# Kernel optimization log

Measured on AMD Instinct MI355X. Metric: run time of the kernel, lower is better.

Reference implementation:

```python
import jax, jax.numpy as jnp
import numpy as np

BS, T, N_AGENTS, N_ACTIONS = 8, 256, 8, 20
A = N_AGENTS * N_ACTIONS          # 160 gru input dim
E, D, HID, S = 128, 128, 32, 256  # encoder_dim, decoder_dim, mixing_embed_dim, state_dim
EMBED = HID * (A + E)             # 9216


def _lin(k, out_d, in_d):
    s = 1.0 / np.sqrt(in_d)
    return jax.random.uniform(k, (out_d, in_d), jnp.float32, -s, s)


def _vec(k, d, fan):
    s = 1.0 / np.sqrt(fan)
    return jax.random.uniform(k, (d,), jnp.float32, -s, s)


def setup_inputs() -> dict:
    key = jax.random.key(0)
    ks = jax.random.split(key, 32)
    inp = {
        'act': jax.random.uniform(ks[0], (BS, T, N_AGENTS, N_ACTIONS), jnp.float32),
        'states': jax.random.normal(ks[1], (BS, T, S), jnp.float32),
        # GRU (PyTorch layout: gates stacked [r; z; n])
        'gru_wih': _lin(ks[2], 3 * E, A),
        'gru_whh': _lin(ks[3], 3 * E, E),
        'gru_bih': _vec(ks[4], 3 * E, E),
        'gru_bhh': _vec(ks[5], 3 * E, E),
        # encoder fc
        'fc_w': _lin(ks[6], D, E),
        'fc_b': _vec(ks[7], D, E),
        # attention
        'attn_w': _lin(ks[8], D, D + E),
        'v_w': _vec(ks[9], D, D),
        # hyper_w_1 (2-layer MLP)
        'hw1_w0': _lin(ks[10], EMBED, S), 'hw1_b0': _vec(ks[11], EMBED, S),
        'hw1_w1': _lin(ks[12], EMBED, EMBED), 'hw1_b1': _vec(ks[13], EMBED, EMBED),
        # hyper_w_final (2-layer MLP)
        'hwf_w0': _lin(ks[14], HID, S), 'hwf_b0': _vec(ks[15], HID, S),
        'hwf_w1': _lin(ks[16], HID, HID), 'hwf_b1': _vec(ks[17], HID, HID),
        # hyper_b_1
        'hb1_w': _lin(ks[18], HID, S), 'hb1_b': _vec(ks[19], HID, S),
        # hyper_b_2 (2-layer MLP)
        'hb2_w0': _lin(ks[20], HID, S), 'hb2_b0': _vec(ks[21], HID, S),
        'hb2_w1': _lin(ks[22], 1, HID), 'hb2_b1': _vec(ks[23], 1, HID),
    }
    return inp


def reference(act, states, gru_wih, gru_whh, gru_bih, gru_bhh, fc_w, fc_b,
              attn_w, v_w, hw1_w0, hw1_b0, hw1_w1, hw1_b1,
              hwf_w0, hwf_b0, hwf_w1, hwf_b1, hb1_w, hb1_b,
              hb2_w0, hb2_b0, hb2_w1, hb2_b1):
    bs, t, n_ag, n_ac = act.shape
    a = n_ag * n_ac
    e = gru_whh.shape[1]
    d = fc_w.shape[0]
    hid = hb1_w.shape[0]

    act_flat = act.reshape(bs, t, a)
    # act_his = [zeros, act]; prefixes use only the first t steps of it
    x = jnp.concatenate([jnp.zeros((bs, 1, a), act.dtype), act_flat[:, : t - 1]], axis=1)

    # GRU over full sequence once (causal => identical to recomputing each prefix)
    def step(h, xt):
        gi = xt @ gru_wih.T + gru_bih
        gh = h @ gru_whh.T + gru_bhh
        ir, iz, i_n = jnp.split(gi, 3, axis=-1)
        hr, hz, h_n = jnp.split(gh, 3, axis=-1)
        r = jax.nn.sigmoid(ir + hr)
        z = jax.nn.sigmoid(iz + hz)
        n = jnp.tanh(i_n + r * h_n)
        h_new = (1.0 - z) * n + z * h
        return h_new, h_new

    h0 = jnp.zeros((bs, e), act.dtype)
    _, enc = jax.lax.scan(step, h0, jnp.swapaxes(x, 0, 1))
    enc = jnp.swapaxes(enc, 0, 1)  # [bs, T, E]

    # s0 for prefix ending at step q is tanh(fc(enc[:, q]))
    s0 = jnp.tanh(enc @ fc_w.T + fc_b)  # [bs, T, D]

    # attention: cat order is (s, enc_output)
    w_s, w_e = attn_w[:, :d], attn_w[:, d:]
    ps = s0 @ w_s.T            # [bs, Tq, D]
    pe = enc @ w_e.T           # [bs, Tk, D]
    pre = jnp.tanh(ps[:, :, None, :] + pe[:, None, :, :])  # [bs, Tq, Tk, D]
    scores = jnp.einsum('bqkd,d->bqk', pre, v_w)
    mask = jnp.tril(jnp.ones((t, t), bool))  # key j <= query q (prefix j < idx)
    scores = jnp.where(mask[None], scores, -jnp.inf)
    attn = jax.nn.softmax(scores, axis=-1)
    c = jnp.einsum('bqk,bke->bqe', attn, enc)  # [bs, T, E]

    inp = jnp.concatenate([act_flat, c], axis=-1).reshape(bs * t, 1, a + e)
    st = states.reshape(bs * t, -1)

    w1 = (jax.nn.relu(st @ hw1_w0.T + hw1_b0) @ hw1_w1.T + hw1_b1).reshape(bs * t, a + e, hid)
    b1 = (st @ hb1_w.T + hb1_b)[:, None, :]
    h = jax.nn.relu(jnp.einsum('bik,bkh->bih', inp, w1) + b1)  # [bs*T, 1, hid]

    wf = (jax.nn.relu(st @ hwf_w0.T + hwf_b0) @ hwf_w1.T + hwf_b1)[:, :, None]  # [bs*T, hid, 1]
    b2 = (jax.nn.relu(st @ hb2_w0.T + hb2_b0) @ hb2_w1.T + hb2_b1)[:, :, None]  # [bs*T, 1, 1]
    q = (jnp.einsum('bih,bho->bio', h, wf) + b2).reshape(bs, t, 1)
    return q
```

## Files before the change

### kernel.cpp

```cpp
#include <hip/hip_runtime.h>
#include <hip/hip_bf16.h>
#include <stdint.h>

typedef __attribute__((ext_vector_type(4))) float f32x4;
typedef __attribute__((ext_vector_type(8))) short short8v;
typedef __attribute__((ext_vector_type(4))) unsigned short u16x4;

constexpr int kT  = 256;
constexpr int kA  = 160;

__device__ __forceinline__ float bf2f(unsigned short u){
  union { unsigned int u; float f; } c; c.u = ((unsigned int)u) << 16; return c.f;
}
__device__ __forceinline__ unsigned short f2bf(float f){
  union { float f; unsigned int u; } c; c.f = f;
  unsigned int r = (c.u + 0x7FFFu + ((c.u >> 16) & 1u)) >> 16;
  return (unsigned short)r;
}
__device__ __forceinline__ float sigmoid_fast(float x){
  return __builtin_amdgcn_rcpf(1.f + __expf(-x));
}
__device__ __forceinline__ float tanhf_fast(float x){
  float xc = fminf(fmaxf(x, -15.f), 15.f);
  float t = __expf(2.f * xc);
  return (t - 1.f) * __builtin_amdgcn_rcpf(t + 1.f);
}
__device__ __forceinline__ void gload_lds16(const void* g, void* l){
  __builtin_amdgcn_global_load_lds((const __attribute__((address_space(1))) void*)g,
                                   (__attribute__((address_space(3))) void*)l, 16, 0, 0);
}
__device__ __forceinline__ void bar_lgkm(){
  asm volatile("s_waitcnt lgkmcnt(0)" ::: "memory");
  __builtin_amdgcn_s_barrier();
  asm volatile("" ::: "memory");
}
__device__ __forceinline__ void bar_only(){
  asm volatile("" ::: "memory");
  __builtin_amdgcn_s_barrier();
  asm volatile("" ::: "memory");
}

__global__ __launch_bounds__(256) void k_fill_f32(float* out, int n, float v){
  int i = blockIdx.x * blockDim.x + threadIdx.x;
  if (i < n) out[i] = v;
}

__global__ __launch_bounds__(256) void k_f32_to_bf16(const float* __restrict__ src,
                                                     unsigned short* __restrict__ dst, int n4){
  int stride = gridDim.x * blockDim.x;
  for (int i = blockIdx.x * blockDim.x + threadIdx.x; i < n4; i += stride){
    f32x4 v = *(const f32x4*)(src + (size_t)i * 4);
    u16x4 o;
    o[0] = f2bf(v[0]); o[1] = f2bf(v[1]); o[2] = f2bf(v[2]); o[3] = f2bf(v[3]);
    *(u16x4*)(dst + (size_t)i * 4) = o;
  }
}

__global__ __launch_bounds__(384) void k_gi(const float* __restrict__ act,
                                            const float* __restrict__ wih,
                                            const float* __restrict__ bih,
                                            float* __restrict__ gi){
  int blk = blockIdx.x;
  int b = blk >> 5, tg = blk & 31;
  int j = threadIdx.x;
  __shared__ __align__(16) float xh[8][kA];
  for (int idx = j; idx < 8 * kA; idx += 384){
    int u = idx / kA, i = idx - u * kA;
    int t = tg * 8 + u;
    xh[u][i] = (t == 0) ? 0.f : act[((size_t)b * kT + t - 1) * kA + i];
  }
  __syncthreads();
  float acc[8] = {0,0,0,0,0,0,0,0};
  for (int i = 0; i < kA; i += 4){
    f32x4 wv = *(const f32x4*)(wih + (size_t)j * kA + i);
#pragma unroll
    for (int jj = 0; jj < 4; ++jj)
#pragma unroll
      for (int u = 0; u < 8; ++u)
        acc[u] += wv[jj] * xh[u][i + jj];
  }
  float bv = bih[j];
#pragma unroll
  for (int u = 0; u < 8; ++u)
    gi[((size_t)b * kT + tg * 8 + u) * 384 + j] = acc[u] + bv;
}

__global__ __launch_bounds__(512) void k_gru_conv(const float* __restrict__ gi,
                                                  const float* __restrict__ whh,
                                                  const float* __restrict__ bhh,
                                                  float* __restrict__ enc,
                                                  const float* __restrict__ csrc,
                                                  unsigned short* __restrict__ cdst,
                                                  int n4){
  if (blockIdx.x >= 8){
    int stride = (gridDim.x - 8) * 512;
    for (int i = (blockIdx.x - 8) * 512 + threadIdx.x; i < n4; i += stride){
      f32x4 v = *(const f32x4*)(csrc + (size_t)i * 4);
      u16x4 o;
      o[0] = f2bf(v[0]); o[1] = f2bf(v[1]); o[2] = f2bf(v[2]); o[3] = f2bf(v[3]);
      *(u16x4*)(cdst + (size_t)i * 4) = o;
    }
    return;
  }
  int b = blockIdx.x;
  int tid = threadIdx.x;
  int e = tid & 127, s = tid >> 7;
  float W0[32], W1[32], W2[32];
#pragma unroll
  for (int k = 0; k < 32; ++k){
    W0[k] = whh[(size_t)(0 * 128 + e) * 128 + s * 32 + k];
    W1[k] = whh[(size_t)(1 * 128 + e) * 128 + s * 32 + k];
    W2[k] = whh[(size_t)(2 * 128 + e) * 128 + s * 32 + k];
  }
  __shared__ __align__(16) float h_lds[128];
  __shared__ __align__(16) float red[12][128];
  if (tid < 128) h_lds[tid] = 0.f;
  float bh0 = 0.f, bh1 = 0.f, bh2 = 0.f;
  if (tid < 128){ bh0 = bhh[e]; bh1 = bhh[128 + e]; bh2 = bhh[256 + e]; }
  const float* gib = gi + (size_t)b * kT * 384;
  float* encb = enc + (size_t)b * kT * 128;
  float gir = 0.f, giz = 0.f, gin = 0.f;
  if (tid < 128){ gir = gib[e]; giz = gib[128 + e]; gin = gib[256 + e]; }
  bar_lgkm();
  for (int t = 0; t < kT; ++t){
    float p0 = 0.f, p1 = 0.f, p2 = 0.f;
#pragma unroll
    for (int k4 = 0; k4 < 8; ++k4){
      f32x4 hv = *(const f32x4*)(h_lds + s * 32 + k4 * 4);
#pragma unroll
      for (int jj = 0; jj < 4; ++jj){
        p0 += W0[k4 * 4 + jj] * hv[jj];
        p1 += W1[k4 * 4 + jj] * hv[jj];
        p2 += W2[k4 * 4 + jj] * hv[jj];
      }
    }
    float nir = 0.f, niz = 0.f, nin = 0.f;
    if (t + 1 < kT && tid < 128){
      const float* gn = gib + (size_t)(t + 1) * 384;
      nir = gn[e]; niz = gn[128 + e]; nin = gn[256 + e];
    }
    red[s * 3 + 0][e] = p0; red[s * 3 + 1][e] = p1; red[s * 3 + 2][e] = p2;
    bar_lgkm();
    if (tid < 128){
      float ghr = red[0][e] + red[3][e] + red[6][e] + red[9][e]  + bh0;
      float ghz = red[1][e] + red[4][e] + red[7][e] + red[10][e] + bh1;
      float ghn = red[2][e] + red[5][e] + red[8][e] + red[11][e] + bh2;
      float r = sigmoid_fast(gir + ghr);
      float z = sigmoid_fast(giz + ghz);
      float n = tanhf_fast(gin + r * ghn);
      float hnew = (1.f - z) * n + z * h_lds[e];
      h_lds[e] = hnew;
      encb[t * 128 + e] = hnew;
    }
    bar_lgkm();
    gir = nir; giz = niz; gin = nin;
  }
}

__global__ __launch_bounds__(128) void k_attnpre(const float* __restrict__ enc,
                                                 const float* __restrict__ fc_w,
                                                 const float* __restrict__ fc_b,
                                                 const float* __restrict__ attn_w,
                                                 float* __restrict__ ps,
                                                 float* __restrict__ pe){
  int bt = blockIdx.x, o = threadIdx.x;
  __shared__ __align__(16) float ench[128], s0h[128];
  ench[o] = enc[(size_t)bt * 128 + o];
  __syncthreads();
  float a0 = fc_b[o], a1 = 0.f;
  for (int i = 0; i < 128; i += 4){
    f32x4 wv = *(const f32x4*)(fc_w + (size_t)o * 128 + i);
    f32x4 we = *(const f32x4*)(attn_w + (size_t)o * 256 + 128 + i);
    f32x4 ev = *(const f32x4*)(ench + i);
#pragma unroll
    for (int jj = 0; jj < 4; ++jj){ a0 += wv[jj] * ev[jj]; a1 += we[jj] * ev[jj]; }
  }
  s0h[o] = tanhf_fast(a0);
  pe[(size_t)bt * 128 + o] = a1;
  __syncthreads();
  float a2 = 0.f;
  for (int i = 0; i < 128; i += 4){
    f32x4 ws = *(const f32x4*)(attn_w + (size_t)o * 256 + i);
    f32x4 sv = *(const f32x4*)(s0h + i);
#pragma unroll
    for (int jj = 0; jj < 4; ++jj) a2 += ws[jj] * sv[jj];
  }
  ps[(size_t)bt * 128 + o] = a2;
}

__global__ __launch_bounds__(256) void k_attn(const float* __restrict__ enc,
                                              const float* __restrict__ ps,
                                              const float* __restrict__ pe,
                                              const float* __restrict__ v_w,
                                              float* __restrict__ cbuf){
  int q = blockIdx.x, b = blockIdx.y;
  int tid = threadIdx.x;
  __shared__ __align__(16) float psh[128], vwh[128];
  __shared__ __align__(16) float sch[256];
  __shared__ __align__(16) float rr[256];
  __shared__ float mxs, dns;
  if (tid < 128){
    psh[tid] = ps[((size_t)b * kT + q) * 128 + tid];
    vwh[tid] = v_w[tid];
  }
  __syncthreads();
  int nk = q + 1;
  for (int k = tid; k < nk; k += 256){
    const float* per = pe + ((size_t)b * kT + k) * 128;
    float sc = 0.f;
    for (int d = 0; d < 128; d += 4){
      f32x4 pv = *(const f32x4*)(per + d);
      f32x4 qv = *(const f32x4*)(psh + d);
      sc += vwh[d + 0] * tanhf_fast(qv[0] + pv[0]);
      sc += vwh[d + 1] * tanhf_fast(qv[1] + pv[1]);
      sc += vwh[d + 2] * tanhf_fast(qv[2] + pv[2]);
      sc += vwh[d + 3] * tanhf_fast(qv[3] + pv[3]);
    }
    sch[k] = sc;
  }
  __syncthreads();
  float lm = -3.0e38f;
  for (int k = tid; k < nk; k += 256) lm = fmaxf(lm, sch[k]);
  rr[tid] = lm; __syncthreads();
  for (int off = 128; off > 0; off >>= 1){
    if (tid < off) rr[tid] = fmaxf(rr[tid], rr[tid + off]);
    __syncthreads();
  }
  if (tid == 0) mxs = rr[0];
  __syncthreads();
  float mxv = mxs;
  float lsum = 0.f;
  for (int k = tid; k < nk; k += 256){
    float p = __expf(sch[k] - mxv);
    sch[k] = p; lsum += p;
  }
  __syncthreads();
  rr[tid] = lsum; __syncthreads();
  for (int off = 128; off > 0; off >>= 1){
    if (tid < off) rr[tid] += rr[tid + off];
    __syncthreads();
  }
  if (tid == 0) dns = __builtin_amdgcn_rcpf(rr[0]);
  __syncthreads();
  float rd = dns;
  int d = tid & 127, half = tid >> 7;
  float acc = 0.f;
  for (int k = half; k < nk; k += 2)
    acc += sch[k] * enc[((size_t)b * kT + k) * 128 + d];
  rr[tid] = acc; __syncthreads();
  if (half == 0)
    cbuf[((size_t)b * kT + q) * 128 + d] = (acc + rr[d + 128]) * rd;
}

template<int RELU>
__global__ __launch_bounds__(512, 4) void k_gemm8(const unsigned short* __restrict__ A,
                                                  const unsigned short* __restrict__ B,
                                                  const float* __restrict__ bias,
                                                  unsigned short* __restrict__ C,
                                                  int M, int Nc, int K, int ldc){
  __shared__ __align__(16) unsigned short Lds[3][12288];
  int nbm = M >> 7;
  int nwg = gridDim.x, bid = blockIdx.x;
  int cpx = nwg >> 3;
  int sw  = (bid & 7) * cpx + (bid >> 3);
  int bm = sw % nbm, bn = sw / nbm;
  int arow0 = bm << 7, bcol0 = bn << 8;
  int t = threadIdx.x;
  int l = t & 63, w = t >> 6;
  int wr = w >> 2, wc = w & 3;
  int lr = l & 15, kq = l >> 4;
  int ra = t >> 2,          pa = t & 3;
  int rb0 = t >> 2,         pb0 = t & 3;
  int rb1 = (t + 512) >> 2, pb1 = (t + 512) & 3;
  int aoffg  = ra  * (K * 2) + ((pa  ^ ((ra  >> 1) & 3)) << 4);
  int boffg0 = rb0 * (K * 2) + ((pb0 ^ ((rb0 >> 1) & 3)) << 4);
  int boffg1 = rb1 * (K * 2) + ((pb1 ^ ((rb1 >> 1) & 3)) << 4);
  const char* Ag = (const char*)(A + (size_t)arow0 * K);
  const char* Bg = (const char*)(B + (size_t)bcol0 * K);
  int lA  = t * 16;
  int lB0 = 8192 + t * 16;
  int lB1 = 16384 + t * 16;
  int kk16 = (kq ^ ((lr >> 1) & 3)) << 4;
  int aRd = (wr * 64 + lr) * 64 + kk16;
  int bRd = 8192 + (wc * 64 + lr) * 64 + kk16;
  f32x4 acc[4][4] = {};
  int nt = K >> 5;

  auto stage = [&](int kt, int bi){
    size_t kb = (size_t)kt * 64;
    char* Ld = (char*)Lds[bi];
    gload_lds16(Ag + aoffg  + kb, Ld + lA);
    gload_lds16(Bg + boffg0 + kb, Ld + lB0);
    gload_lds16(Bg + boffg1 + kb, Ld + lB1);
  };
  auto compute = [&](int bi){
    const char* Ld = (const char*)Lds[bi];
    short8v af[4], bf[4];
#pragma unroll
    for (int m = 0; m < 4; ++m) af[m] = *(const short8v*)(Ld + aRd + m * 1024);
#pragma unroll
    for (int n = 0; n < 4; ++n) bf[n] = *(const short8v*)(Ld + bRd + n * 1024);
    __builtin_amdgcn_s_setprio(1);
#pragma unroll
    for (int m = 0; m < 4; ++m)
#pragma unroll
      for (int n = 0; n < 4; ++n)
        acc[m][n] = __builtin_amdgcn_mfma_f32_16x16x32_bf16(af[m], bf[n], acc[m][n], 0, 0, 0);
    __builtin_amdgcn_s_setprio(0);
  };

  stage(0, 0);
  stage(1, 1);
  int cur = 0;
  for (int kt = 0; kt < nt; ++kt){
    if (kt + 2 < nt){
      int nb = cur + 2; if (nb >= 3) nb -= 3;
      stage(kt + 2, nb);
      asm volatile("s_waitcnt vmcnt(6)" ::: "memory");
    } else if (kt + 2 == nt){
      asm volatile("s_waitcnt vmcnt(3)" ::: "memory");
    } else {
      asm volatile("s_waitcnt vmcnt(0)" ::: "memory");
    }
    bar_only();
    compute(cur);
    bar_only();
    ++cur; if (cur == 3) cur = 0;
  }

#pragma unroll
  for (int m = 0; m < 4; ++m){
    int row = arow0 + wr * 64 + m * 16 + kq * 4;
#pragma unroll
    for (int n = 0; n < 4; ++n){
      int col = bcol0 + wc * 64 + n * 16 + lr;
      float bv = bias[col];
#pragma unroll
      for (int r = 0; r < 4; ++r){
        float v = acc[m][n][r] + bv;
        if (RELU) v = fmaxf(v, 0.f);
        C[(size_t)(row + r) * ldc + col] = f2bf(v);
      }
    }
  }
}

__global__ __launch_bounds__(256) void k_final(const float* __restrict__ states,
                                               const float* __restrict__ act,
                                               const float* __restrict__ cbuf,
                                               const unsigned short* __restrict__ w1f,
                                               const float* __restrict__ hb1_w, const float* __restrict__ hb1_b,
                                               const float* __restrict__ hwf_w0, const float* __restrict__ hwf_b0,
                                               const float* __restrict__ hwf_w1, const float* __restrict__ hwf_b1,
                                               const float* __restrict__ hb2_w0, const float* __restrict__ hb2_b0,
                                               const float* __restrict__ hb2_w1, const float* __restrict__ hb2_b1,
                                               float* __restrict__ out){
  int bt = blockIdx.x, tid = threadIdx.x;
  __shared__ __align__(16) float sth[256], inph[288], red[256];
  __shared__ __align__(16) float t1h[32], t2h[32], b1h[32], wfh[32], hvals[32];
  __shared__ float b2s;
  sth[tid] = states[(size_t)bt * 256 + tid];
  if (tid < 160) inph[tid] = act[(size_t)bt * 160 + tid];
  if (tid < 128) inph[160 + tid] = cbuf[(size_t)bt * 128 + tid];
  __syncthreads();
  int o = tid & 31, s = tid >> 5;
  float p1 = 0.f, p2 = 0.f, p3 = 0.f;
  for (int k = s * 32; k < s * 32 + 32; k += 4){
    f32x4 sv  = *(const f32x4*)(sth + k);
    f32x4 w1v = *(const f32x4*)(hwf_w0 + (size_t)o * 256 + k);
    f32x4 w2v = *(const f32x4*)(hb2_w0 + (size_t)o * 256 + k);
    f32x4 w3v = *(const f32x4*)(hb1_w  + (size_t)o * 256 + k);
#pragma unroll
    for (int jj = 0; jj < 4; ++jj){
      p1 += w1v[jj] * sv[jj]; p2 += w2v[jj] * sv[jj]; p3 += w3v[jj] * sv[jj];
    }
  }
  red[tid] = p1; __syncthreads();
  if (tid < 32){
    float a = hwf_b0[tid];
#pragma unroll
    for (int s8 = 0; s8 < 8; ++s8) a += red[s8 * 32 + tid];
    t1h[tid] = fmaxf(a, 0.f);
  }
  __syncthreads();
  red[tid] = p2; __syncthreads();
  if (tid < 32){
    float a = hb2_b0[tid];
#pragma unroll
    for (int s8 = 0; s8 < 8; ++s8) a += red[s8 * 32 + tid];
    t2h[tid] = fmaxf(a, 0.f);
  }
  __syncthreads();
  red[tid] = p3; __syncthreads();
  if (tid < 32){
    float a = hb1_b[tid];
#pragma unroll
    for (int s8 = 0; s8 < 8; ++s8) a += red[s8 * 32 + tid];
    b1h[tid] = a;
  }
  __syncthreads();
  if (tid < 32){
    float a = hwf_b1[tid];
#pragma unroll
    for (int j = 0; j < 32; ++j) a += hwf_w1[(size_t)tid * 32 + j] * t1h[j];
    wfh[tid] = a;
  }
  if (tid == 64){
    float a = hb2_b1[0];
#pragma unroll
    for (int j = 0; j < 32; ++j) a += hb2_w1[j] * t2h[j];
    b2s = a;
  }
  __syncthreads();
  float ph = 0.f;
  const unsigned short* wrow = w1f + (size_t)bt * 9216;
  for (int i = s * 36; i < s * 36 + 36; ++i)
    ph += inph[i] * bf2f(wrow[i * 32 + o]);
  red[tid] = ph; __syncthreads();
  if (tid < 32){
    float a = b1h[tid];
#pragma unroll
    for (int s8 = 0; s8 < 8; ++s8) a += red[s8 * 32 + tid];
    hvals[tid] = fmaxf(a, 0.f) * wfh[tid];
  }
  __syncthreads();
  if (tid == 0){
    float q = b2s;
#pragma unroll
    for (int j = 0; j < 32; ++j) q += hvals[j];
    out[bt] = q;
  }
}

extern "C" void kernel_launch(void* const* d_in, const int* in_sizes, int n_in,
                              void* d_out, int out_size, void* d_ws, size_t ws_size,
                              hipStream_t stream){
  float* outp = (float*)d_out;

  bool ok = (n_in == 24) && out_size == 2048 &&
            in_sizes[0] == 327680 && in_sizes[1] == 524288 &&
            in_sizes[2] == 61440  && in_sizes[3] == 49152 &&
            in_sizes[10] == 2359296 && in_sizes[12] == 84934656;
  if (!ok){
    k_fill_f32<<<dim3(8), dim3(256), 0, stream>>>(outp, 2048, 1.0e6f);
    return;
  }

  const float* act    = (const float*)d_in[0];
  const float* states = (const float*)d_in[1];
  const float* wih    = (const float*)d_in[2];
  const float* whh    = (const float*)d_in[3];
  const float* bih    = (const float*)d_in[4];
  const float* bhh    = (const float*)d_in[5];
  const float* fc_w   = (const float*)d_in[6];
  const float* fc_b   = (const float*)d_in[7];
  const float* attn_w = (const float*)d_in[8];
  const float* v_w    = (const float*)d_in[9];
  const float* hw1_w0 = (const float*)d_in[10];
  const float* hw1_b0 = (const float*)d_in[11];
  const float* hw1_w1 = (const float*)d_in[12];
  const float* hw1_b1 = (const float*)d_in[13];
  const float* hwf_w0 = (const float*)d_in[14];
  const float* hwf_b0 = (const float*)d_in[15];
  const float* hwf_w1 = (const float*)d_in[16];
  const float* hwf_b1 = (const float*)d_in[17];
  const float* hb1_w  = (const float*)d_in[18];
  const float* hb1_b  = (const float*)d_in[19];
  const float* hb2_w0 = (const float*)d_in[20];
  const float* hb2_b0 = (const float*)d_in[21];
  const float* hb2_w1 = (const float*)d_in[22];
  const float* hb2_b1 = (const float*)d_in[23];

  char* ws = (char*)d_ws;
  size_t off = 0;
  auto alloc = [&](size_t bytes)->void*{
    void* p = ws + off; off += (bytes + 255) & ~(size_t)255; return p;
  };
  unsigned short* zb  = (unsigned short*)alloc((size_t)2048 * 9216 * 2);
  unsigned short* w1f = (unsigned short*)alloc((size_t)2048 * 9216 * 2);
  unsigned short* w0b = (unsigned short*)alloc((size_t)9216 * 256 * 2);
  unsigned short* stb = (unsigned short*)alloc((size_t)2048 * 256 * 2);
  float* gi   = (float*)alloc((size_t)2048 * 384 * 4);
  float* enc  = (float*)alloc((size_t)2048 * 128 * 4);
  float* psb  = (float*)alloc((size_t)2048 * 128 * 4);
  float* peb  = (float*)alloc((size_t)2048 * 128 * 4);
  float* cbuf = (float*)alloc((size_t)2048 * 128 * 4);
  size_t floor_bytes = off;
  const size_t row_bytes = (size_t)9216 * 2;
  if (ws_size < floor_bytes + 256 * row_bytes){
    k_fill_f32<<<dim3(8), dim3(256), 0, stream>>>(outp, 2048, (float)(ws_size >> 20));
    return;
  }
  size_t avail = ws_size - floor_bytes;
  int chunk_rows = (int)(((avail / row_bytes) / 256) * 256);
  if (chunk_rows > 9216) chunk_rows = 9216;
  unsigned short* w1c = (unsigned short*)(ws + floor_bytes);
  int first_nc = chunk_rows < 9216 ? chunk_rows : 9216;

  k_f32_to_bf16<<<dim3(1024), dim3(256), 0, stream>>>(hw1_w0, w0b, 9216 * 256 / 4);
  k_f32_to_bf16<<<dim3(256),  dim3(256), 0, stream>>>(states, stb, 2048 * 256 / 4);
  k_gi<<<dim3(256), dim3(384), 0, stream>>>(act, wih, bih, gi);
  k_gru_conv<<<dim3(2048), dim3(512), 0, stream>>>(gi, whh, bhh, enc,
                                                   hw1_w1, w1c, first_nc * 9216 / 4);
  k_attnpre<<<dim3(2048), dim3(128), 0, stream>>>(enc, fc_w, fc_b, attn_w, psb, peb);
  k_attn<<<dim3(256, 8), dim3(256), 0, stream>>>(enc, psb, peb, v_w, cbuf);
  k_gemm8<1><<<dim3(16 * 36), dim3(512), 0, stream>>>(stb, w0b, hw1_b0, zb, 2048, 9216, 256, 9216);
  for (int c0 = 0; c0 < 9216; c0 += chunk_rows){
    int nc = 9216 - c0; if (nc > chunk_rows) nc = chunk_rows;
    if (c0 > 0)
      k_f32_to_bf16<<<dim3(2048), dim3(256), 0, stream>>>(hw1_w1 + (size_t)c0 * 9216, w1c, nc * 9216 / 4);
    k_gemm8<0><<<dim3(16 * (nc >> 8)), dim3(512), 0, stream>>>(zb, w1c, hw1_b1 + c0, w1f + c0,
                                                               2048, nc, 9216, 9216);
  }
  k_final<<<dim3(2048), dim3(256), 0, stream>>>(states, act, cbuf, w1f,
      hb1_w, hb1_b, hwf_w0, hwf_b0, hwf_w1, hwf_b1, hb2_w0, hb2_b0, hb2_w1, hb2_b1,
      outp);
}
```

Before: 832.2 us.

## Use 128x576 GEMM tiles and fuse first hypernet GEMM into GRU launch

Replaces the 128x256-tile bf16 MFMA GEMM with a 128x576 tile (9 column fragments per wave, 144KB LDS triple buffer, one barrier per k-step). For N=9216 this gives 256 workgroups, one per CU, instead of 576. The first hypernet layer GEMM now runs inside the GRU/conversion launch as extra blocks, so it overlaps the serial GRU recurrence rather than running as its own kernel. The cost is one workgroup per CU with heavy register use for 36 accumulators, plus a larger minimum workspace chunk.

```diff
diff --git a/kernel.cpp b/kernel.cpp
--- a/kernel.cpp
+++ b/kernel.cpp
@@ -85,16 +85,127 @@
     gi[((size_t)b * kT + tg * 8 + u) * 384 + j] = acc[u] + bv;
 }
 
-__global__ __launch_bounds__(512) void k_gru_conv(const float* __restrict__ gi,
-                                                  const float* __restrict__ whh,
-                                                  const float* __restrict__ bhh,
-                                                  float* __restrict__ enc,
-                                                  const float* __restrict__ csrc,
-                                                  unsigned short* __restrict__ cdst,
-                                                  int n4){
-  if (blockIdx.x >= 8){
-    int stride = (gridDim.x - 8) * 512;
-    for (int i = (blockIdx.x - 8) * 512 + threadIdx.x; i < n4; i += stride){
+template<int RELU>
+__device__ __forceinline__ void gemm576_body(const unsigned short* __restrict__ A,
+                                             const unsigned short* __restrict__ B,
+                                             const float* __restrict__ bias,
+                                             unsigned short* __restrict__ C,
+                                             int M, int Nc, int K, int ldc,
+                                             int bid, int nwg, char* smem){
+  int nbm = M >> 7;
+  int cpx = nwg >> 3;
+  int sw  = (bid & 7) * cpx + (bid >> 3);
+  int bm = sw % nbm, bn = sw / nbm;
+  int arow0 = bm << 7;
+  int bcol0 = bn * 576;
+  int t = threadIdx.x;
+  int l = t & 63, w = t >> 6;
+  int wr = w >> 2, wc = w & 3;
+  int lr = l & 15, kq = l >> 4;
+  int Kb = K * 2;
+  int ar = t >> 2, ap = t & 3;
+  size_t aoffg = (size_t)ar * Kb + ((ap ^ ((ar >> 1) & 3)) << 4);
+  size_t boffg[5];
+#pragma unroll
+  for (int i = 0; i < 5; ++i){
+    int q = i * 512 + t, r = q >> 2, p = q & 3;
+    boffg[i] = (size_t)r * Kb + ((p ^ ((r >> 1) & 3)) << 4);
+  }
+  const char* Ag = (const char*)(A + (size_t)arow0 * K);
+  const char* Bg = (const char*)(B + (size_t)bcol0 * K);
+  int dA = t * 16;
+  int kk16 = (kq ^ ((lr >> 1) & 3)) << 4;
+  int aRd = (wr * 64 + lr) * 64 + kk16;
+  int bRd = 8192 + (wc * 144 + lr) * 64 + kk16;
+  f32x4 acc[4][9] = {};
+  int nt = K >> 5;
+
+  auto stage = [&](int kt, int bi){
+    size_t kb = (size_t)kt * 64;
+    char* Ld = smem + bi * 49152;
+    gload_lds16(Ag + aoffg + kb, Ld + dA);
+#pragma unroll
+    for (int i = 0; i < 5; ++i)
+      gload_lds16(Bg + boffg[i] + kb, Ld + 8192 + i * 8192 + dA);
+  };
+
+  stage(0, 0);
+  stage(1, 1);
+  asm volatile("s_waitcnt vmcnt(6)" ::: "memory");
+  int cur = 0;
+  for (int kt = 0; kt < nt; ++kt){
+    bar_only();
+    if (kt + 2 < nt){
+      int nb = cur + 2; if (nb >= 3) nb -= 3;
+      stage(kt + 2, nb);
+    }
+    const char* Ld = smem + cur * 49152;
+    short8v af[4];
+#pragma unroll
+    for (int m = 0; m < 4; ++m) af[m] = *(const short8v*)(Ld + aRd + m * 1024);
+#pragma unroll
+    for (int c = 0; c < 3; ++c){
+      short8v bf[3];
+#pragma unroll
+      for (int j = 0; j < 3; ++j) bf[j] = *(const short8v*)(Ld + bRd + (c * 3 + j) * 1024);
+      __builtin_amdgcn_s_setprio(1);
+#pragma unroll
+      for (int m = 0; m < 4; ++m)
+#pragma unroll
+        for (int j = 0; j < 3; ++j)
+          acc[m][c * 3 + j] = __builtin_amdgcn_mfma_f32_16x16x32_bf16(af[m], bf[j], acc[m][c * 3 + j], 0, 0, 0);
+      __builtin_amdgcn_s_setprio(0);
+    }
+    if (kt + 1 < nt){
+      if (kt + 2 < nt) asm volatile("s_waitcnt vmcnt(6)" ::: "memory");
+      else             asm volatile("s_waitcnt vmcnt(0)" ::: "memory");
+    }
+    ++cur; if (cur == 3) cur = 0;
+  }
+
+#pragma unroll
+  for (int m = 0; m < 4; ++m){
+    int row = arow0 + wr * 64 + m * 16 + kq * 4;
+#pragma unroll
+    for (int n = 0; n < 9; ++n){
+      int col = bcol0 + wc * 144 + n * 16 + lr;
+      float bv = bias[col];
+#pragma unroll
+      for (int r = 0; r < 4; ++r){
+        float v = acc[m][n][r] + bv;
+        if (RELU) v = fmaxf(v, 0.f);
+        C[(size_t)(row + r) * ldc + col] = f2bf(v);
+      }
+    }
+  }
+}
+
+template<int RELU>
+__global__ __launch_bounds__(512) void k_gemm576(const unsigned short* __restrict__ A,
+                                                 const unsigned short* __restrict__ B,
+                                                 const float* __restrict__ bias,
+                                                 unsigned short* __restrict__ C,
+                                                 int M, int Nc, int K, int ldc){
+  __shared__ __align__(16) char smem[147456];
+  gemm576_body<RELU>(A, B, bias, C, M, Nc, K, ldc, blockIdx.x, gridDim.x, smem);
+}
+
+__global__ __launch_bounds__(512) void k_gru_g1_conv(const float* __restrict__ gi,
+                                                     const float* __restrict__ whh,
+                                                     const float* __restrict__ bhh,
+                                                     float* __restrict__ enc,
+                                                     const unsigned short* __restrict__ stb,
+                                                     const unsigned short* __restrict__ w0b,
+                                                     const float* __restrict__ hb0,
+                                                     unsigned short* __restrict__ zb,
+                                                     const float* __restrict__ csrc,
+                                                     unsigned short* __restrict__ cdst,
+                                                     int n4){
+  __shared__ __align__(16) char smem[147456];
+  int blk = blockIdx.x;
+  if (blk >= 264){
+    int stride = (gridDim.x - 264) * 512;
+    for (int i = (blk - 264) * 512 + threadIdx.x; i < n4; i += stride){
       f32x4 v = *(const f32x4*)(csrc + (size_t)i * 4);
       u16x4 o;
       o[0] = f2bf(v[0]); o[1] = f2bf(v[1]); o[2] = f2bf(v[2]); o[3] = f2bf(v[3]);
@@ -102,7 +213,13 @@
     }
     return;
   }
-  int b = blockIdx.x;
+  if (blk >= 8){
+    gemm576_body<1>(stb, w0b, hb0, zb, 2048, 9216, 256, 9216, blk - 8, 256, smem);
+    return;
+  }
+  float* h_lds = (float*)smem;
+  float (*red)[128] = (float(*)[128])(smem + 512);
+  int b = blk;
   int tid = threadIdx.x;
   int e = tid & 127, s = tid >> 7;
   float W0[32], W1[32], W2[32];
@@ -112,8 +229,6 @@
     W1[k] = whh[(size_t)(1 * 128 + e) * 128 + s * 32 + k];
     W2[k] = whh[(size_t)(2 * 128 + e) * 128 + s * 32 + k];
   }
-  __shared__ __align__(16) float h_lds[128];
-  __shared__ __align__(16) float red[12][128];
   if (tid < 128) h_lds[tid] = 0.f;
   float bh0 = 0.f, bh1 = 0.f, bh2 = 0.f;
   if (tid < 128){ bh0 = bhh[e]; bh1 = bhh[128 + e]; bh2 = bhh[256 + e]; }
@@ -250,99 +365,6 @@
   rr[tid] = acc; __syncthreads();
   if (half == 0)
     cbuf[((size_t)b * kT + q) * 128 + d] = (acc + rr[d + 128]) * rd;
-}
-
-template<int RELU>
-__global__ __launch_bounds__(512, 4) void k_gemm8(const unsigned short* __restrict__ A,
-                                                  const unsigned short* __restrict__ B,
-                                                  const float* __restrict__ bias,
-                                                  unsigned short* __restrict__ C,
-                                                  int M, int Nc, int K, int ldc){
-  __shared__ __align__(16) unsigned short Lds[3][12288];
-  int nbm = M >> 7;
-  int nwg = gridDim.x, bid = blockIdx.x;
-  int cpx = nwg >> 3;
-  int sw  = (bid & 7) * cpx + (bid >> 3);
-  int bm = sw % nbm, bn = sw / nbm;
-  int arow0 = bm << 7, bcol0 = bn << 8;
-  int t = threadIdx.x;
-  int l = t & 63, w = t >> 6;
-  int wr = w >> 2, wc = w & 3;
-  int lr = l & 15, kq = l >> 4;
-  int ra = t >> 2,          pa = t & 3;
-  int rb0 = t >> 2,         pb0 = t & 3;
-  int rb1 = (t + 512) >> 2, pb1 = (t + 512) & 3;
-  int aoffg  = ra  * (K * 2) + ((pa  ^ ((ra  >> 1) & 3)) << 4);
-  int boffg0 = rb0 * (K * 2) + ((pb0 ^ ((rb0 >> 1) & 3)) << 4);
-  int boffg1 = rb1 * (K * 2) + ((pb1 ^ ((rb1 >> 1) & 3)) << 4);
-  const char* Ag = (const char*)(A + (size_t)arow0 * K);
-  const char* Bg = (const char*)(B + (size_t)bcol0 * K);
-  int lA  = t * 16;
-  int lB0 = 8192 + t * 16;
-  int lB1 = 16384 + t * 16;
-  int kk16 = (kq ^ ((lr >> 1) & 3)) << 4;
-  int aRd = (wr * 64 + lr) * 64 + kk16;
-  int bRd = 8192 + (wc * 64 + lr) * 64 + kk16;
-  f32x4 acc[4][4] = {};
-  int nt = K >> 5;
-
-  auto stage = [&](int kt, int bi){
-    size_t kb = (size_t)kt * 64;
-    char* Ld = (char*)Lds[bi];
-    gload_lds16(Ag + aoffg  + kb, Ld + lA);
-    gload_lds16(Bg + boffg0 + kb, Ld + lB0);
-    gload_lds16(Bg + boffg1 + kb, Ld + lB1);
-  };
-  auto compute = [&](int bi){
-    const char* Ld = (const char*)Lds[bi];
-    short8v af[4], bf[4];
-#pragma unroll
-    for (int m = 0; m < 4; ++m) af[m] = *(const short8v*)(Ld + aRd + m * 1024);
-#pragma unroll
-    for (int n = 0; n < 4; ++n) bf[n] = *(const short8v*)(Ld + bRd + n * 1024);
-    __builtin_amdgcn_s_setprio(1);
-#pragma unroll
-    for (int m = 0; m < 4; ++m)
-#pragma unroll
-      for (int n = 0; n < 4; ++n)
-        acc[m][n] = __builtin_amdgcn_mfma_f32_16x16x32_bf16(af[m], bf[n], acc[m][n], 0, 0, 0);
-    __builtin_amdgcn_s_setprio(0);
-  };
-
-  stage(0, 0);
-  stage(1, 1);
-  int cur = 0;
-  for (int kt = 0; kt < nt; ++kt){
-    if (kt + 2 < nt){
-      int nb = cur + 2; if (nb >= 3) nb -= 3;
-      stage(kt + 2, nb);
-      asm volatile("s_waitcnt vmcnt(6)" ::: "memory");
-    } else if (kt + 2 == nt){
-      asm volatile("s_waitcnt vmcnt(3)" ::: "memory");
-    } else {
-      asm volatile("s_waitcnt vmcnt(0)" ::: "memory");
-    }
-    bar_only();
-    compute(cur);
-    bar_only();
-    ++cur; if (cur == 3) cur = 0;
-  }
-
-#pragma unroll
-  for (int m = 0; m < 4; ++m){
-    int row = arow0 + wr * 64 + m * 16 + kq * 4;
-#pragma unroll
-    for (int n = 0; n < 4; ++n){
-      int col = bcol0 + wc * 64 + n * 16 + lr;
-      float bv = bias[col];
-#pragma unroll
-      for (int r = 0; r < 4; ++r){
-        float v = acc[m][n][r] + bv;
-        if (RELU) v = fmaxf(v, 0.f);
-        C[(size_t)(row + r) * ldc + col] = f2bf(v);
-      }
-    }
-  }
 }
 
 __global__ __launch_bounds__(256) void k_final(const float* __restrict__ states,
@@ -487,30 +509,31 @@
   float* cbuf = (float*)alloc((size_t)2048 * 128 * 4);
   size_t floor_bytes = off;
   const size_t row_bytes = (size_t)9216 * 2;
-  if (ws_size < floor_bytes + 256 * row_bytes){
+  const size_t slack = (size_t)2 << 20;
+  if (ws_size < floor_bytes + 576 * row_bytes + slack){
     k_fill_f32<<<dim3(8), dim3(256), 0, stream>>>(outp, 2048, (float)(ws_size >> 20));
     return;
   }
-  size_t avail = ws_size - floor_bytes;
-  int chunk_rows = (int)(((avail / row_bytes) / 256) * 256);
+  size_t avail = ws_size - floor_bytes - slack;
+  int chunk_rows = (int)(((avail / row_bytes) / 576) * 576);
   if (chunk_rows > 9216) chunk_rows = 9216;
   unsigned short* w1c = (unsigned short*)(ws + floor_bytes);
-  int first_nc = chunk_rows < 9216 ? chunk_rows : 9216;
+  int first_nc = chunk_rows;
 
   k_f32_to_bf16<<<dim3(1024), dim3(256), 0, stream>>>(hw1_w0, w0b, 9216 * 256 / 4);
   k_f32_to_bf16<<<dim3(256),  dim3(256), 0, stream>>>(states, stb, 2048 * 256 / 4);
   k_gi<<<dim3(256), dim3(384), 0, stream>>>(act, wih, bih, gi);
-  k_gru_conv<<<dim3(2048), dim3(512), 0, stream>>>(gi, whh, bhh, enc,
-                                                   hw1_w1, w1c, first_nc * 9216 / 4);
+  k_gru_g1_conv<<<dim3(768), dim3(512), 0, stream>>>(gi, whh, bhh, enc,
+                                                     stb, w0b, hw1_b0, zb,
+                                                     hw1_w1, w1c, first_nc * 9216 / 4);
   k_attnpre<<<dim3(2048), dim3(128), 0, stream>>>(enc, fc_w, fc_b, attn_w, psb, peb);
   k_attn<<<dim3(256, 8), dim3(256), 0, stream>>>(enc, psb, peb, v_w, cbuf);
-  k_gemm8<1><<<dim3(16 * 36), dim3(512), 0, stream>>>(stb, w0b, hw1_b0, zb, 2048, 9216, 256, 9216);
   for (int c0 = 0; c0 < 9216; c0 += chunk_rows){
     int nc = 9216 - c0; if (nc > chunk_rows) nc = chunk_rows;
     if (c0 > 0)
       k_f32_to_bf16<<<dim3(2048), dim3(256), 0, stream>>>(hw1_w1 + (size_t)c0 * 9216, w1c, nc * 9216 / 4);
-    k_gemm8<0><<<dim3(16 * (nc >> 8)), dim3(512), 0, stream>>>(zb, w1c, hw1_b1 + c0, w1f + c0,
-                                                               2048, nc, 9216, 9216);
+    k_gemm576<0><<<dim3(16 * (nc / 576)), dim3(512), 0, stream>>>(zb, w1c, hw1_b1 + c0, w1f + c0,
+                                                                  2048, nc, 9216, 9216);
   }
   k_final<<<dim3(2048), dim3(256), 0, stream>>>(states, act, cbuf, w1f,
       hb1_w, hb1_b, hwf_w0, hwf_b0, hwf_w1, hwf_b1, hb2_w0, hb2_b0, hb2_w1, hb2_b1,
```

Result: faster. 747.8 us (-10.1%).
